# Kernel optimization log

Hardware: AMD Instinct MI355X
Metric: run time of the kernel (lower is better)

Reference implementation:

```python
import jax, jax.numpy as jnp
import numpy as np

NUM_HEADS = 16
FOCUS_FACTOR = 1.6
HEAD_REGION = {0: 0, 1: 1, 2: 2}  # head -> region (first/middle/end)


def setup_inputs() -> dict:
    key = jax.random.key(0)
    k1, k2, k3, k4, k5 = jax.random.split(key, 5)
    B, S, D = 2, 2048, 1024
    # GPT-2 style init scale so softmax is not fully saturated
    return {
        "hidden_states": jax.random.normal(k1, (B, S, D), dtype=jnp.float32),
        "c_attn_w": jax.random.normal(k2, (D, 3 * D), dtype=jnp.float32) * 0.02,
        "c_attn_b": jax.random.normal(k3, (3 * D,), dtype=jnp.float32) * 0.02,
        "c_proj_w": jax.random.normal(k4, (D, D), dtype=jnp.float32) * 0.02,
        "c_proj_b": jax.random.normal(k5, (D,), dtype=jnp.float32) * 0.02,
    }


def _region_multipliers(seq_len: int, num_heads: int, factor: float) -> jnp.ndarray:
    """[H, S] multiplier: selected heads up-weight their token region."""
    first_end = max(1, seq_len // 3)
    second_end = max(first_end + 1, 2 * seq_len // 3)
    pos = jnp.arange(seq_len)
    regions = [
        pos < first_end,
        (pos >= first_end) & (pos < second_end),
        pos >= second_end,
    ]
    mult = np.ones((num_heads, seq_len), dtype=np.float32)
    mult = jnp.asarray(mult)
    for h, r in HEAD_REGION.items():
        if h < num_heads:
            mult = mult.at[h].set(1.0 + (factor - 1.0) * regions[r].astype(jnp.float32))
    return mult


def reference(hidden_states, c_attn_w, c_attn_b, c_proj_w, c_proj_b):
    B, S, D = hidden_states.shape
    H = NUM_HEADS
    hd = D // H

    qkv = hidden_states @ c_attn_w + c_attn_b  # [B, S, 3D]
    q, k, v = jnp.split(qkv, 3, axis=-1)

    def _reshape(x):  # [B, S, D] -> [B, H, S, hd]
        return x.reshape(B, S, H, hd).transpose(0, 2, 1, 3)

    q, k, v = _reshape(q), _reshape(k), _reshape(v)

    scores = jnp.einsum("bhqd,bhkd->bhqk", q, k) / jnp.sqrt(jnp.float32(hd))
    causal = jnp.tril(jnp.ones((S, S), dtype=bool))
    mask_value = jnp.finfo(scores.dtype).min
    scores = jnp.where(causal[None, None], scores, mask_value)

    attn = jax.nn.softmax(scores, axis=-1)  # [B, H, S, S]

    # Per-head region reweight + renorm (only for the divergent heads)
    mult = _region_multipliers(S, H, FOCUS_FACTOR)  # [H, S]
    scaled = attn * mult[None, :, None, :]
    scaled = scaled / jnp.sum(scaled, axis=-1, keepdims=True)
    div_heads = jnp.zeros((H,), dtype=bool)
    for h in HEAD_REGION:
        if h < H:
            div_heads = div_heads.at[h].set(True)
    attn = jnp.where(div_heads[None, :, None, None], scaled, attn)

    out = jnp.einsum("bhqk,bhkd->bhqd", attn, v)  # [B, H, S, hd]
    out = out.transpose(0, 2, 1, 3).reshape(B, S, D)
    out = out @ c_proj_w + c_proj_b
    return out
```

## Files before the change

### kernel.cpp

```cpp
#include <hip/hip_runtime.h>
#include <hip/hip_bf16.h>

typedef __attribute__((ext_vector_type(8))) short bf16x8;
typedef __attribute__((ext_vector_type(4))) float f32x4;
typedef __attribute__((ext_vector_type(16))) float f32x16;
typedef __attribute__((ext_vector_type(4))) unsigned int u32x4;
typedef unsigned short u16;

#define MFMA_BF16(a, b, c) __builtin_amdgcn_mfma_f32_16x16x32_bf16(a, b, c, 0, 0, 0)
#define MFMA32(a, b, c) __builtin_amdgcn_mfma_f32_32x32x16_bf16(a, b, c, 0, 0, 0)

__device__ inline u16 f2b(float x) {
  unsigned int u = __builtin_bit_cast(unsigned int, x);
  u += 0x7fffu + ((u >> 16) & 1u);
  return (u16)(u >> 16);
}

__device__ inline float exp2_fast(float x) {
  float r;
  asm("v_exp_f32 %0, %1" : "=v"(r) : "v"(x));
  return r;
}

__device__ inline unsigned int cvtpk_bf16(float lo, float hi) {
  unsigned int r;
  asm("v_cvt_pk_bf16_f32 %0, %1, %2" : "=v"(r) : "v"(lo), "v"(hi));
  return r;
}

__device__ inline void pswap(unsigned int& dst, unsigned int& src) {
  asm("v_permlane32_swap_b32 %0, %1" : "+v"(dst), "+v"(src));
}

__device__ inline void gload16(void* lds, const void* g) {
  __builtin_amdgcn_global_load_lds((const __attribute__((address_space(1))) void*)g,
                                   (__attribute__((address_space(3))) void*)lds,
                                   16, 0, 0);
}


__global__ __launch_bounds__(256) void cast_f32_bf16(const float* __restrict__ src,
                                                     u16* __restrict__ dst, int n4) {
  int i = blockIdx.x * blockDim.x + threadIdx.x;
  if (i < n4) {
    float4 v = ((const float4*)src)[i];
    ushort4 o;
    o.x = f2b(v.x); o.y = f2b(v.y); o.z = f2b(v.z); o.w = f2b(v.w);
    ((ushort4*)dst)[i] = o;
  }
}

__global__ __launch_bounds__(256) void transpose_cast(const float* __restrict__ src,
                                                      u16* __restrict__ dst, int K, int N) {
  __shared__ float t[32][33];
  int k0 = blockIdx.x * 32, n0 = blockIdx.y * 32;
  int tx = threadIdx.x, ty = threadIdx.y;
#pragma unroll
  for (int i = 0; i < 4; i++) t[ty + i * 8][tx] = src[(size_t)(k0 + ty + i * 8) * N + n0 + tx];
  __syncthreads();
#pragma unroll
  for (int i = 0; i < 4; i++)
    dst[(size_t)(n0 + ty + i * 8) * K + k0 + tx] = f2b(t[tx][ty + i * 8]);
}

#define QSCALE 0.1803368801f

__global__ __launch_bounds__(512, 2) void gemm256_qkv(
    const u16* __restrict__ A, const u16* __restrict__ BT, const float* __restrict__ bias,
    u16* __restrict__ oQ, u16* __restrict__ oK, u16* __restrict__ oVf) {
  __shared__ __align__(16) u16 As[2][256 * 64];
  __shared__ __align__(16) u16 Bs[2][256 * 64];
  const int K = 1024, NT = 16;
  int tid = threadIdx.x;
  int wv = tid >> 6, lane = tid & 63, lr = lane & 15, lg = lane >> 4;
  int wm = wv >> 2, wn = wv & 3;
  int bx = blockIdx.x % 12, by = blockIdx.x / 12;
  int m0 = by * 256, n0 = bx * 256;
  const int swz = (lr & 7) << 4;

  f32x4 acc[8][4] = {};

  auto stageA = [&](int buf, int kt, int h) {
#pragma unroll
    for (int g = 0; g < 2; g++) {
      int li = g * 512 + tid;
      int row = (li >> 3) + h * 128;
      int cb = ((li & 7) * 16) ^ ((row & 7) << 4);
      gload16((char*)&As[buf][0] + h * 16384 + g * 8192 + wv * 1024,
              (const char*)(A + (size_t)(m0 + row) * K + kt * 64) + cb);
    }
  };
  auto stageB = [&](int buf, int kt, int h) {
#pragma unroll
    for (int g = 0; g < 2; g++) {
      int li = g * 512 + tid;
      int row = (li >> 3) + h * 128;
      int cb = ((li & 7) * 16) ^ ((row & 7) << 4);
      gload16((char*)&Bs[buf][0] + h * 16384 + g * 8192 + wv * 1024,
              (const char*)(BT + (size_t)(n0 + row) * K + kt * 64) + cb);
    }
  };

  stageA(0, 0, 0);
  stageB(0, 0, 0);
  stageA(0, 0, 1);
  stageB(0, 0, 1);

  for (int t = 0; t < NT; ++t) {
    const int buf = t & 1;
    const bool last = (t == NT - 1);
#pragma unroll
    for (int p = 0; p < 4; p++) {
      const int Mq = p & 1, Nq = p >> 1;
      if (last) {
        if (p == 0) asm volatile("s_waitcnt vmcnt(0)" ::: "memory");
      } else if (p < 3) {
        asm volatile("s_waitcnt vmcnt(4)" ::: "memory");
      }
      __builtin_amdgcn_s_barrier();
      bf16x8 a[4][2], b[2][2];
#pragma unroll
      for (int ii = 0; ii < 4; ii++) {
        int row = wm * 16 + ii * 32 + Mq * 128 + lr;
#pragma unroll
        for (int kk = 0; kk < 2; kk++)
          a[ii][kk] = *(const bf16x8*)((const char*)&As[buf][0] + row * 128 +
                                       ((kk * 64 + lg * 16) ^ swz));
      }
#pragma unroll
      for (int jj2 = 0; jj2 < 2; jj2++) {
        int row = wn * 16 + jj2 * 64 + Nq * 128 + lr;
#pragma unroll
        for (int kk = 0; kk < 2; kk++)
          b[jj2][kk] = *(const bf16x8*)((const char*)&Bs[buf][0] + row * 128 +
                                        ((kk * 64 + lg * 16) ^ swz));
      }
      if (!last) {
        if (p == 0) stageA(buf ^ 1, t + 1, 0);
        else if (p == 1) stageB(buf ^ 1, t + 1, 0);
        else if (p == 2) stageA(buf ^ 1, t + 1, 1);
        else stageB(buf ^ 1, t + 1, 1);
      }
      __builtin_amdgcn_s_setprio(1);
#pragma unroll
      for (int ii = 0; ii < 4; ii++)
#pragma unroll
        for (int jj2 = 0; jj2 < 2; jj2++)
#pragma unroll
          for (int kk = 0; kk < 2; kk++)
            acc[Mq * 4 + ii][Nq * 2 + jj2] =
                MFMA_BF16(a[ii][kk], b[jj2][kk], acc[Mq * 4 + ii][Nq * 2 + jj2]);
      __builtin_amdgcn_s_setprio(0);
    }
  }

#pragma unroll
  for (int i = 0; i < 8; i++) {
#pragma unroll
    for (int j = 0; j < 4; j++) {
#pragma unroll
      for (int jj = 0; jj < 4; jj++) {
        int row = m0 + wm * 16 + (i & 3) * 32 + (i >> 2) * 128 + lg * 4 + jj;
        int col = n0 + wn * 16 + (j & 1) * 64 + (j >> 1) * 128 + lr;
        float v = acc[i][j][jj] + bias[col];
        int bb = row >> 11, s = row & 2047;
        int tile = s >> 6, key = s & 63;
        if (col < 1024) {
          oQ[((size_t)((bb * 16 + (col >> 6)) * 2048 + s)) * 64 + (col & 63)] = f2b(v * QSCALE);
        } else if (col < 2048) {
          int c = col - 1024;
          int hh = c >> 6, d = c & 63;
          int jf = ((key >> 5) << 2) + (d >> 4);
          int ln = (((d >> 3) & 1) << 5) | (key & 31);
          oK[(size_t)(bb * 16 + hh) * 131072 + tile * 4096 + jf * 512 + ln * 8 + (d & 7)] =
              f2b(v);
        } else {
          int c = col - 2048;
          int hh = c >> 6, d = c & 63;
          int jf = ((d >> 5) << 2) + (key >> 4);
          int ln = (((key >> 3) & 1) << 5) | (d & 31);
          oVf[(size_t)(bb * 16 + hh) * 131072 + tile * 4096 + jf * 512 + ln * 8 + (key & 7)] =
              f2b(v);
        }
      }
    }
  }
}

__global__ __launch_bounds__(256) void gemm_bt_f32(
    const u16* __restrict__ A, const u16* __restrict__ BT, const float* __restrict__ bias,
    float* __restrict__ oF, int M, int N, int K, int nbx) {
  __shared__ __align__(16) u16 As[128 * 64];
  __shared__ __align__(16) u16 Bs[128 * 64];
  int tid = threadIdx.x;
  int wv = tid >> 6, lane = tid & 63, lr = lane & 15, lg = lane >> 4;
  int bx = blockIdx.x % nbx, by = blockIdx.x / nbx;
  int m0 = by * 128, n0 = bx * 128;
  int wr = (wv >> 1) * 64, wc = (wv & 1) * 64;

  f32x4 acc[4][4] = {};

  for (int k0 = 0; k0 < K; k0 += 64) {
#pragma unroll
    for (int j = 0; j < 4; j++) {
      int li = j * 256 + tid;
      int row = li >> 3;
      int cb = ((li & 7) * 16) ^ ((row & 7) << 4);
      gload16((char*)As + j * 4096 + wv * 1024,
              (const char*)(A + (size_t)(m0 + row) * K + k0) + cb);
      gload16((char*)Bs + j * 4096 + wv * 1024,
              (const char*)(BT + (size_t)(n0 + row) * K + k0) + cb);
    }
    __syncthreads();
#pragma unroll
    for (int kk = 0; kk < 2; kk++) {
      bf16x8 a[4], b[4];
#pragma unroll
      for (int i = 0; i < 4; i++) {
        int row = wr + i * 16 + lr;
        a[i] = *(const bf16x8*)((const char*)As + row * 128 +
                                ((kk * 64 + lg * 16) ^ ((row & 7) << 4)));
      }
#pragma unroll
      for (int j = 0; j < 4; j++) {
        int row = wc + j * 16 + lr;
        b[j] = *(const bf16x8*)((const char*)Bs + row * 128 +
                                ((kk * 64 + lg * 16) ^ ((row & 7) << 4)));
      }
#pragma unroll
      for (int i = 0; i < 4; i++)
#pragma unroll
        for (int j = 0; j < 4; j++) acc[i][j] = MFMA_BF16(a[i], b[j], acc[i][j]);
    }
    __syncthreads();
  }

#pragma unroll
  for (int i = 0; i < 4; i++)
#pragma unroll
    for (int j = 0; j < 4; j++)
#pragma unroll
      for (int jj = 0; jj < 4; jj++) {
        int row = m0 + wr + i * 16 + lg * 4 + jj;
        int col = n0 + wc + j * 16 + lr;
        oF[(size_t)row * N + col] = acc[i][j][jj] + bias[col];
      }
}

#define SEQL 2048
#define FIRST_END 682
#define SECOND_END 1365
#define LOG2F16 0.6780719051f

__global__ __launch_bounds__(256) void attn_kernel(const u16* __restrict__ Qb,
                                                   const u16* __restrict__ Kf,
                                                   const u16* __restrict__ Vf,
                                                   u16* __restrict__ AO) {
  __shared__ float Ol[4][16][66];
  __shared__ float Ml[4][32], Ll[4][32], Cl[4][32];

  int tid = threadIdx.x;
  int w = tid >> 6, l = tid & 63;
  int r31 = l & 31, hi = l >> 5;

  int xcd = blockIdx.x & 7, slot = blockIdx.x >> 3;
  int bh = xcd * 4 + (slot >> 6);
  int qt = 63 - (slot & 63);
  int q0 = qt * 32;
  int h = bh & 15, b = bh >> 4;

  const u16* Qp = Qb + ((size_t)bh * SEQL + q0 + r31) * 64 + hi * 8;
  bf16x8 qa[4];
#pragma unroll
  for (int kb = 0; kb < 4; kb++) qa[kb] = *(const bf16x8*)(Qp + kb * 16);

  const u16* Kfp = Kf + (size_t)bh * 131072;
  const u16* Vfp = Vf + (size_t)bh * 131072;

  f32x16 o0 = {}, o1 = {};
  float m = -1e30f, lsum = 0.f;

  const int N = (q0 + 95) >> 6;
  const bool hasb = (h < 3);

  for (int t = w; t < N; t += 4) {
    const int kv0 = t << 6;
    const bool last = (t == N - 1);
    const u16* kt = Kfp + (size_t)t * 4096;
    const u16* vt = Vfp + (size_t)t * 4096;

    bf16x8 ka[4], kb2[4];
#pragma unroll
    for (int kb = 0; kb < 4; kb++) {
      ka[kb]  = *(const bf16x8*)(kt + kb * 512 + l * 8);
      kb2[kb] = *(const bf16x8*)(kt + (4 + kb) * 512 + l * 8);
    }
    f32x16 sA = {}, sB = {};
#pragma unroll
    for (int kb = 0; kb < 4; kb++) sA = MFMA32(ka[kb], qa[kb], sA);
#pragma unroll
    for (int kb = 0; kb < 4; kb++) sB = MFMA32(kb2[kb], qa[kb], sB);

    if (hasb) {
#pragma unroll
      for (int r = 0; r < 16; r++) {
        int kA = kv0 + ((r & 3) + 8 * (r >> 2) + 4 * hi);
        int kB = kA + 32;
        int rA = (kA < FIRST_END) ? 0 : (kA < SECOND_END) ? 1 : 2;
        int rB = (kB < FIRST_END) ? 0 : (kB < SECOND_END) ? 1 : 2;
        if (rA == h) sA[r] += LOG2F16;
        if (rB == h) sB[r] += LOG2F16;
      }
    }
    if (last) {
      int q = q0 + r31;
#pragma unroll
      for (int r = 0; r < 16; r++) {
        int kA = kv0 + ((r & 3) + 8 * (r >> 2) + 4 * hi);
        if (kA > q) sA[r] = -1e30f;
        if (kA + 32 > q) sB[r] = -1e30f;
      }
    }

#define MAX4(v, i) fmaxf(fmaxf(v[i], v[i + 1]), fmaxf(v[i + 2], v[i + 3]))
    float mA = fmaxf(fmaxf(MAX4(sA, 0), MAX4(sA, 4)), fmaxf(MAX4(sA, 8), MAX4(sA, 12)));
    float mB = fmaxf(fmaxf(MAX4(sB, 0), MAX4(sB, 4)), fmaxf(MAX4(sB, 8), MAX4(sB, 12)));
    float mx = fmaxf(mA, mB);
    mx = fmaxf(mx, __shfl_xor(mx, 32));
    float mn = fmaxf(m, mx);
    float corr = exp2_fast(m - mn);
    m = mn;

    unsigned int wA[8], wB[8];
    float s0 = 0.f, s1 = 0.f;
#pragma unroll
    for (int i = 0; i < 8; i++) {
      float pa0 = exp2_fast(sA[2 * i] - mn), pa1 = exp2_fast(sA[2 * i + 1] - mn);
      float pb0 = exp2_fast(sB[2 * i] - mn), pb1 = exp2_fast(sB[2 * i + 1] - mn);
      s0 += pa0 + pa1;
      s1 += pb0 + pb1;
      wA[i] = cvtpk_bf16(pa0, pa1);
      wB[i] = cvtpk_bf16(pb0, pb1);
    }
    float ssum = s0 + s1;
    ssum += __shfl_xor(ssum, 32);
    lsum = lsum * corr + ssum;
    o0 *= corr;
    o1 *= corr;

    pswap(wA[0], wA[2]); pswap(wA[1], wA[3]);
    pswap(wA[4], wA[6]); pswap(wA[5], wA[7]);
    pswap(wB[0], wB[2]); pswap(wB[1], wB[3]);
    pswap(wB[4], wB[6]); pswap(wB[5], wB[7]);

    bf16x8 pb[4];
    pb[0] = __builtin_bit_cast(bf16x8, (u32x4){wA[0], wA[1], wA[2], wA[3]});
    pb[1] = __builtin_bit_cast(bf16x8, (u32x4){wA[4], wA[5], wA[6], wA[7]});
    pb[2] = __builtin_bit_cast(bf16x8, (u32x4){wB[0], wB[1], wB[2], wB[3]});
    pb[3] = __builtin_bit_cast(bf16x8, (u32x4){wB[4], wB[5], wB[6], wB[7]});

#pragma unroll
    for (int c = 0; c < 4; c++) {
      bf16x8 va0 = *(const bf16x8*)(vt + c * 512 + l * 8);
      bf16x8 va1 = *(const bf16x8*)(vt + (4 + c) * 512 + l * 8);
      o0 = MFMA32(va0, pb[c], o0);
      o1 = MFMA32(va1, pb[c], o1);
    }
  }

  Ml[w][r31] = m;
  Ll[w][r31] = lsum;
#pragma unroll
  for (int r = 0; r < 16; r++) Ol[w][r][l] = o0[r];
  __syncthreads();

  if (tid < 128) {
    int w2 = tid >> 5, q = tid & 31;
    float m0 = Ml[0][q], m1 = Ml[1][q], m2 = Ml[2][q], m3 = Ml[3][q];
    float ms = fmaxf(fmaxf(m0, m1), fmaxf(m2, m3));
    float e0 = exp2_fast(m0 - ms), e1 = exp2_fast(m1 - ms);
    float e2 = exp2_fast(m2 - ms), e3 = exp2_fast(m3 - ms);
    float ls = Ll[0][q] * e0 + Ll[1][q] * e1 + Ll[2][q] * e2 + Ll[3][q] * e3;
    float ei = (w2 == 0) ? e0 : (w2 == 1) ? e1 : (w2 == 2) ? e2 : e3;
    Cl[w2][q] = ei / ls;
  }
  __syncthreads();

  int mq = tid >> 3, md = (tid & 7) * 4;
  float c0 = Cl[0][mq], c1 = Cl[1][mq], c2 = Cl[2][mq], c3 = Cl[3][mq];
  u16* aop = AO + ((size_t)(b * SEQL + q0 + mq)) * 1024 + h * 64;

  {
    u16 ov[4];
#pragma unroll
    for (int j = 0; j < 4; j++) {
      int d = md + j;
      int h2 = (d >> 2) & 1, rr = (d & 3) + 4 * (d >> 3);
      int ll2 = mq + 32 * h2;
      ov[j] = f2b(Ol[0][rr][ll2] * c0 + Ol[1][rr][ll2] * c1 +
                  Ol[2][rr][ll2] * c2 + Ol[3][rr][ll2] * c3);
    }
    *(uint2*)(aop + md) = *(const uint2*)ov;
  }
  __syncthreads();
#pragma unroll
  for (int r = 0; r < 16; r++) Ol[w][r][l] = o1[r];
  __syncthreads();
  {
    u16 ov[4];
#pragma unroll
    for (int j = 0; j < 4; j++) {
      int d = md + j;
      int h2 = (d >> 2) & 1, rr = (d & 3) + 4 * (d >> 3);
      int ll2 = mq + 32 * h2;
      ov[j] = f2b(Ol[0][rr][ll2] * c0 + Ol[1][rr][ll2] * c1 +
                  Ol[2][rr][ll2] * c2 + Ol[3][rr][ll2] * c3);
    }
    *(uint2*)(aop + 32 + md) = *(const uint2*)ov;
  }
}


extern "C" void kernel_launch(void* const* d_in, const int* in_sizes, int n_in,
                              void* d_out, int out_size, void* d_ws, size_t ws_size,
                              hipStream_t stream) {
  const float* hs = (const float*)d_in[0];
  const float* w1 = (const float*)d_in[1];
  const float* b1 = (const float*)d_in[2];
  const float* w2 = (const float*)d_in[3];
  const float* b2 = (const float*)d_in[4];
  float* out = (float*)d_out;

  char* ws = (char*)d_ws;
  const size_t MB = 1u << 20;
  u16* hsb = (u16*)(ws + 0);
  u16* w1t = (u16*)(ws + 8 * MB);
  u16* w2t = (u16*)(ws + 14 * MB);
  u16* Qb = (u16*)(ws + 16 * MB);
  u16* Kf = (u16*)(ws + 24 * MB);
  u16* Vf = (u16*)(ws + 32 * MB);
  u16* AO = hsb;

  cast_f32_bf16<<<4096, 256, 0, stream>>>(hs, hsb, 4096 * 1024 / 4);
  dim3 tb(32, 8);
  transpose_cast<<<dim3(32, 96), tb, 0, stream>>>(w1, w1t, 1024, 3072);
  transpose_cast<<<dim3(32, 32), tb, 0, stream>>>(w2, w2t, 1024, 1024);

  gemm256_qkv<<<16 * 12, 512, 0, stream>>>(hsb, w1t, b1, Qb, Kf, Vf);
  attn_kernel<<<2048, 256, 0, stream>>>(Qb, Kf, Vf, AO);
  gemm_bt_f32<<<32 * 8, 256, 0, stream>>>(AO, w2t, b2, out, 4096, 1024, 1024, 8);
}
```

Before: 130.6 us.

## Share double-buffered LDS K/V tiles across four query waves in attention

Each attention block now covers 128 queries, one 32-query slice per wave, instead of 32 queries with the KV range split across waves. K/V tiles are staged into a double-buffered LDS area with direct global-to-LDS loads, so all four waves reuse each tile and the next tile is prefetched during compute. This removes the cross-wave softmax merge through shared memory and lets each wave write its normalized output directly. The trade-off is four times fewer blocks and waves, longer serial KV loops per wave, and barrier-induced idling from causal imbalance between waves in the same block.

```diff
diff --git a/kernel.cpp b/kernel.cpp
--- a/kernel.cpp
+++ b/kernel.cpp
@@ -252,21 +252,21 @@
 #define SECOND_END 1365
 #define LOG2F16 0.6780719051f
 
-__global__ __launch_bounds__(256) void attn_kernel(const u16* __restrict__ Qb,
-                                                   const u16* __restrict__ Kf,
-                                                   const u16* __restrict__ Vf,
-                                                   u16* __restrict__ AO) {
-  __shared__ float Ol[4][16][66];
-  __shared__ float Ml[4][32], Ll[4][32], Cl[4][32];
+__global__ __launch_bounds__(256, 2) void attn_kernel(const u16* __restrict__ Qb,
+                                                      const u16* __restrict__ Kf,
+                                                      const u16* __restrict__ Vf,
+                                                      u16* __restrict__ AO) {
+  __shared__ __align__(16) char KV[2][16384];
 
   int tid = threadIdx.x;
   int w = tid >> 6, l = tid & 63;
   int r31 = l & 31, hi = l >> 5;
 
   int xcd = blockIdx.x & 7, slot = blockIdx.x >> 3;
-  int bh = xcd * 4 + (slot >> 6);
-  int qt = 63 - (slot & 63);
-  int q0 = qt * 32;
+  int bh = xcd * 4 + (slot & 3);
+  int qb = 15 - (slot >> 2);
+  int q0B = qb * 128;
+  int q0 = q0B + w * 32;
   int h = bh & 15, b = bh >> 4;
 
   const u16* Qp = Qb + ((size_t)bh * SEQL + q0 + r31) * 64 + hi * 8;
@@ -274,149 +274,134 @@
 #pragma unroll
   for (int kb = 0; kb < 4; kb++) qa[kb] = *(const bf16x8*)(Qp + kb * 16);
 
-  const u16* Kfp = Kf + (size_t)bh * 131072;
-  const u16* Vfp = Vf + (size_t)bh * 131072;
+  const char* Ktg = (const char*)(Kf + (size_t)bh * 131072);
+  const char* Vtg = (const char*)(Vf + (size_t)bh * 131072);
 
   f32x16 o0 = {}, o1 = {};
   float m = -1e30f, lsum = 0.f;
 
-  const int N = (q0 + 95) >> 6;
+  const int nsteps_w = (q0 + 95) >> 6;
+  const int nsteps_blk = (q0B + 191) >> 6;
   const bool hasb = (h < 3);
 
-  for (int t = w; t < N; t += 4) {
-    const int kv0 = t << 6;
-    const bool last = (t == N - 1);
-    const u16* kt = Kfp + (size_t)t * 4096;
-    const u16* vt = Vfp + (size_t)t * 4096;
-
-    bf16x8 ka[4], kb2[4];
-#pragma unroll
-    for (int kb = 0; kb < 4; kb++) {
-      ka[kb]  = *(const bf16x8*)(kt + kb * 512 + l * 8);
-      kb2[kb] = *(const bf16x8*)(kt + (4 + kb) * 512 + l * 8);
-    }
-    f32x16 sA = {}, sB = {};
-#pragma unroll
-    for (int kb = 0; kb < 4; kb++) sA = MFMA32(ka[kb], qa[kb], sA);
-#pragma unroll
-    for (int kb = 0; kb < 4; kb++) sB = MFMA32(kb2[kb], qa[kb], sB);
-
-    if (hasb) {
-#pragma unroll
-      for (int r = 0; r < 16; r++) {
-        int kA = kv0 + ((r & 3) + 8 * (r >> 2) + 4 * hi);
-        int kB = kA + 32;
-        int rA = (kA < FIRST_END) ? 0 : (kA < SECOND_END) ? 1 : 2;
-        int rB = (kB < FIRST_END) ? 0 : (kB < SECOND_END) ? 1 : 2;
-        if (rA == h) sA[r] += LOG2F16;
-        if (rB == h) sB[r] += LOG2F16;
-      }
-    }
-    if (last) {
-      int q = q0 + r31;
-#pragma unroll
-      for (int r = 0; r < 16; r++) {
-        int kA = kv0 + ((r & 3) + 8 * (r >> 2) + 4 * hi);
-        if (kA > q) sA[r] = -1e30f;
-        if (kA + 32 > q) sB[r] = -1e30f;
-      }
-    }
+  auto stage = [&](int buf, int t) {
+    const char* ks = Ktg + (size_t)t * 8192;
+    const char* vs = Vtg + (size_t)t * 8192;
+#pragma unroll
+    for (int r = 0; r < 2; r++) {
+      gload16(&KV[buf][r * 4096 + w * 1024], ks + r * 4096 + w * 1024 + l * 16);
+      gload16(&KV[buf][8192 + r * 4096 + w * 1024], vs + r * 4096 + w * 1024 + l * 16);
+    }
+  };
+
+  stage(0, 0);
+  asm volatile("s_waitcnt vmcnt(0)" ::: "memory");
+  __builtin_amdgcn_s_barrier();
+
+  for (int t = 0; t < nsteps_blk; ++t) {
+    const int cur = t & 1;
+    if (t + 1 < nsteps_blk) stage(cur ^ 1, t + 1);
+
+    if (t < nsteps_w) {
+      const int kv0 = t << 6;
+      const bool last = (t == nsteps_w - 1);
+      const char* kt = &KV[cur][0];
+      const char* vt = &KV[cur][8192];
+
+      bf16x8 ka[4], kb2[4];
+#pragma unroll
+      for (int kb = 0; kb < 4; kb++) {
+        ka[kb]  = *(const bf16x8*)(kt + kb * 1024 + l * 16);
+        kb2[kb] = *(const bf16x8*)(kt + (4 + kb) * 1024 + l * 16);
+      }
+      f32x16 sA = {}, sB = {};
+#pragma unroll
+      for (int kb = 0; kb < 4; kb++) sA = MFMA32(ka[kb], qa[kb], sA);
+#pragma unroll
+      for (int kb = 0; kb < 4; kb++) sB = MFMA32(kb2[kb], qa[kb], sB);
+
+      if (hasb) {
+#pragma unroll
+        for (int r = 0; r < 16; r++) {
+          int kA = kv0 + ((r & 3) + 8 * (r >> 2) + 4 * hi);
+          int kB = kA + 32;
+          int rA = (kA < FIRST_END) ? 0 : (kA < SECOND_END) ? 1 : 2;
+          int rB = (kB < FIRST_END) ? 0 : (kB < SECOND_END) ? 1 : 2;
+          if (rA == h) sA[r] += LOG2F16;
+          if (rB == h) sB[r] += LOG2F16;
+        }
+      }
+      if (last) {
+        int q = q0 + r31;
+#pragma unroll
+        for (int r = 0; r < 16; r++) {
+          int kA = kv0 + ((r & 3) + 8 * (r >> 2) + 4 * hi);
+          if (kA > q) sA[r] = -1e30f;
+          if (kA + 32 > q) sB[r] = -1e30f;
+        }
+      }
 
 #define MAX4(v, i) fmaxf(fmaxf(v[i], v[i + 1]), fmaxf(v[i + 2], v[i + 3]))
-    float mA = fmaxf(fmaxf(MAX4(sA, 0), MAX4(sA, 4)), fmaxf(MAX4(sA, 8), MAX4(sA, 12)));
-    float mB = fmaxf(fmaxf(MAX4(sB, 0), MAX4(sB, 4)), fmaxf(MAX4(sB, 8), MAX4(sB, 12)));
-    float mx = fmaxf(mA, mB);
-    mx = fmaxf(mx, __shfl_xor(mx, 32));
-    float mn = fmaxf(m, mx);
-    float corr = exp2_fast(m - mn);
-    m = mn;
-
-    unsigned int wA[8], wB[8];
-    float s0 = 0.f, s1 = 0.f;
-#pragma unroll
-    for (int i = 0; i < 8; i++) {
-      float pa0 = exp2_fast(sA[2 * i] - mn), pa1 = exp2_fast(sA[2 * i + 1] - mn);
-      float pb0 = exp2_fast(sB[2 * i] - mn), pb1 = exp2_fast(sB[2 * i + 1] - mn);
-      s0 += pa0 + pa1;
-      s1 += pb0 + pb1;
-      wA[i] = cvtpk_bf16(pa0, pa1);
-      wB[i] = cvtpk_bf16(pb0, pb1);
-    }
-    float ssum = s0 + s1;
-    ssum += __shfl_xor(ssum, 32);
-    lsum = lsum * corr + ssum;
-    o0 *= corr;
-    o1 *= corr;
-
-    pswap(wA[0], wA[2]); pswap(wA[1], wA[3]);
-    pswap(wA[4], wA[6]); pswap(wA[5], wA[7]);
-    pswap(wB[0], wB[2]); pswap(wB[1], wB[3]);
-    pswap(wB[4], wB[6]); pswap(wB[5], wB[7]);
-
-    bf16x8 pb[4];
-    pb[0] = __builtin_bit_cast(bf16x8, (u32x4){wA[0], wA[1], wA[2], wA[3]});
-    pb[1] = __builtin_bit_cast(bf16x8, (u32x4){wA[4], wA[5], wA[6], wA[7]});
-    pb[2] = __builtin_bit_cast(bf16x8, (u32x4){wB[0], wB[1], wB[2], wB[3]});
-    pb[3] = __builtin_bit_cast(bf16x8, (u32x4){wB[4], wB[5], wB[6], wB[7]});
-
-#pragma unroll
-    for (int c = 0; c < 4; c++) {
-      bf16x8 va0 = *(const bf16x8*)(vt + c * 512 + l * 8);
-      bf16x8 va1 = *(const bf16x8*)(vt + (4 + c) * 512 + l * 8);
-      o0 = MFMA32(va0, pb[c], o0);
-      o1 = MFMA32(va1, pb[c], o1);
-    }
-  }
-
-  Ml[w][r31] = m;
-  Ll[w][r31] = lsum;
-#pragma unroll
-  for (int r = 0; r < 16; r++) Ol[w][r][l] = o0[r];
-  __syncthreads();
-
-  if (tid < 128) {
-    int w2 = tid >> 5, q = tid & 31;
-    float m0 = Ml[0][q], m1 = Ml[1][q], m2 = Ml[2][q], m3 = Ml[3][q];
-    float ms = fmaxf(fmaxf(m0, m1), fmaxf(m2, m3));
-    float e0 = exp2_fast(m0 - ms), e1 = exp2_fast(m1 - ms);
-    float e2 = exp2_fast(m2 - ms), e3 = exp2_fast(m3 - ms);
-    float ls = Ll[0][q] * e0 + Ll[1][q] * e1 + Ll[2][q] * e2 + Ll[3][q] * e3;
-    float ei = (w2 == 0) ? e0 : (w2 == 1) ? e1 : (w2 == 2) ? e2 : e3;
-    Cl[w2][q] = ei / ls;
-  }
-  __syncthreads();
-
-  int mq = tid >> 3, md = (tid & 7) * 4;
-  float c0 = Cl[0][mq], c1 = Cl[1][mq], c2 = Cl[2][mq], c3 = Cl[3][mq];
-  u16* aop = AO + ((size_t)(b * SEQL + q0 + mq)) * 1024 + h * 64;
-
-  {
-    u16 ov[4];
-#pragma unroll
-    for (int j = 0; j < 4; j++) {
-      int d = md + j;
-      int h2 = (d >> 2) & 1, rr = (d & 3) + 4 * (d >> 3);
-      int ll2 = mq + 32 * h2;
-      ov[j] = f2b(Ol[0][rr][ll2] * c0 + Ol[1][rr][ll2] * c1 +
-                  Ol[2][rr][ll2] * c2 + Ol[3][rr][ll2] * c3);
-    }
-    *(uint2*)(aop + md) = *(const uint2*)ov;
-  }
-  __syncthreads();
-#pragma unroll
-  for (int r = 0; r < 16; r++) Ol[w][r][l] = o1[r];
-  __syncthreads();
-  {
-    u16 ov[4];
-#pragma unroll
-    for (int j = 0; j < 4; j++) {
-      int d = md + j;
-      int h2 = (d >> 2) & 1, rr = (d & 3) + 4 * (d >> 3);
-      int ll2 = mq + 32 * h2;
-      ov[j] = f2b(Ol[0][rr][ll2] * c0 + Ol[1][rr][ll2] * c1 +
-                  Ol[2][rr][ll2] * c2 + Ol[3][rr][ll2] * c3);
-    }
-    *(uint2*)(aop + 32 + md) = *(const uint2*)ov;
+      float mA = fmaxf(fmaxf(MAX4(sA, 0), MAX4(sA, 4)), fmaxf(MAX4(sA, 8), MAX4(sA, 12)));
+      float mB = fmaxf(fmaxf(MAX4(sB, 0), MAX4(sB, 4)), fmaxf(MAX4(sB, 8), MAX4(sB, 12)));
+      float mx = fmaxf(mA, mB);
+      mx = fmaxf(mx, __shfl_xor(mx, 32));
+      float mn = fmaxf(m, mx);
+      float corr = exp2_fast(m - mn);
+      m = mn;
+
+      unsigned int wA[8], wB[8];
+      float s0 = 0.f, s1 = 0.f;
+#pragma unroll
+      for (int i = 0; i < 8; i++) {
+        float pa0 = exp2_fast(sA[2 * i] - mn), pa1 = exp2_fast(sA[2 * i + 1] - mn);
+        float pb0 = exp2_fast(sB[2 * i] - mn), pb1 = exp2_fast(sB[2 * i + 1] - mn);
+        s0 += pa0 + pa1;
+        s1 += pb0 + pb1;
+        wA[i] = cvtpk_bf16(pa0, pa1);
+        wB[i] = cvtpk_bf16(pb0, pb1);
+      }
+      float ssum = s0 + s1;
+      ssum += __shfl_xor(ssum, 32);
+      lsum = lsum * corr + ssum;
+      o0 *= corr;
+      o1 *= corr;
+
+      pswap(wA[0], wA[2]); pswap(wA[1], wA[3]);
+      pswap(wA[4], wA[6]); pswap(wA[5], wA[7]);
+      pswap(wB[0], wB[2]); pswap(wB[1], wB[3]);
+      pswap(wB[4], wB[6]); pswap(wB[5], wB[7]);
+
+      bf16x8 pb[4];
+      pb[0] = __builtin_bit_cast(bf16x8, (u32x4){wA[0], wA[1], wA[2], wA[3]});
+      pb[1] = __builtin_bit_cast(bf16x8, (u32x4){wA[4], wA[5], wA[6], wA[7]});
+      pb[2] = __builtin_bit_cast(bf16x8, (u32x4){wB[0], wB[1], wB[2], wB[3]});
+      pb[3] = __builtin_bit_cast(bf16x8, (u32x4){wB[4], wB[5], wB[6], wB[7]});
+
+#pragma unroll
+      for (int c = 0; c < 4; c++) {
+        bf16x8 va0 = *(const bf16x8*)(vt + c * 1024 + l * 16);
+        bf16x8 va1 = *(const bf16x8*)(vt + (4 + c) * 1024 + l * 16);
+        o0 = MFMA32(va0, pb[c], o0);
+        o1 = MFMA32(va1, pb[c], o1);
+      }
+    }
+
+    asm volatile("s_waitcnt vmcnt(0)" ::: "memory");
+    __builtin_amdgcn_s_barrier();
+  }
+
+  float inv = 1.0f / lsum;
+  u16* aop = AO + ((size_t)(b * SEQL + q0 + r31)) * 1024 + h * 64;
+#pragma unroll
+  for (int dt = 0; dt < 2; dt++) {
+    const f32x16& o = dt ? o1 : o0;
+#pragma unroll
+    for (int r = 0; r < 16; r += 2) {
+      int d = dt * 32 + (r & 3) + 8 * (r >> 2) + 4 * hi;
+      unsigned int wo = (unsigned int)f2b(o[r] * inv) | ((unsigned int)f2b(o[r + 1] * inv) << 16);
+      *(unsigned int*)(aop + d) = wo;
+    }
   }
 }
 
@@ -447,6 +432,6 @@
   transpose_cast<<<dim3(32, 32), tb, 0, stream>>>(w2, w2t, 1024, 1024);
 
   gemm256_qkv<<<16 * 12, 512, 0, stream>>>(hsb, w1t, b1, Qb, Kf, Vf);
-  attn_kernel<<<2048, 256, 0, stream>>>(Qb, Kf, Vf, AO);
+  attn_kernel<<<512, 256, 0, stream>>>(Qb, Kf, Vf, AO);
   gemm_bt_f32<<<32 * 8, 256, 0, stream>>>(AO, w2t, b2, out, 4096, 1024, 1024, 8);
 }
```

Measured after the change: 146.3 us. 1.12x slower.

## Switch QKV GEMM to 32x32x16 MFMA with two-phase staging schedule

Applied to the files above, without the earlier changes.

Rewrites the 256x256 QKV projection GEMM inner loop to use 32x32x16 bf16 MFMA tiles instead of 16x16x32, so each wave holds 4x2 blocks of 32x32 accumulators. The k-loop now has two barrier phases per tile instead of four, and global prefetch of the next tile is interleaved between MFMA groups in a new order (A0, B0, B1, A1). The larger MFMA shape raises operand reuse per LDS read and cuts barrier count. The epilogue index mapping is changed to match the 32x32 accumulator layout, and the waitcnt thresholds are retuned for the new load order, which carries some risk of ordering mistakes.

```diff
diff --git a/kernel.cpp b/kernel.cpp
--- a/kernel.cpp
+++ b/kernel.cpp
@@ -72,13 +72,13 @@
   __shared__ __align__(16) u16 Bs[2][256 * 64];
   const int K = 1024, NT = 16;
   int tid = threadIdx.x;
-  int wv = tid >> 6, lane = tid & 63, lr = lane & 15, lg = lane >> 4;
+  int wv = tid >> 6, lane = tid & 63;
+  int r31 = lane & 31, hi = lane >> 5;
   int wm = wv >> 2, wn = wv & 3;
   int bx = blockIdx.x % 12, by = blockIdx.x / 12;
   int m0 = by * 256, n0 = bx * 256;
-  const int swz = (lr & 7) << 4;
-
-  f32x4 acc[8][4] = {};
+
+  f32x16 acc[4][2] = {};
 
   auto stageA = [&](int buf, int kt, int h) {
 #pragma unroll
@@ -103,66 +103,87 @@
 
   stageA(0, 0, 0);
   stageB(0, 0, 0);
+  stageB(0, 0, 1);
   stageA(0, 0, 1);
-  stageB(0, 0, 1);
 
   for (int t = 0; t < NT; ++t) {
     const int buf = t & 1;
     const bool last = (t == NT - 1);
-#pragma unroll
-    for (int p = 0; p < 4; p++) {
-      const int Mq = p & 1, Nq = p >> 1;
-      if (last) {
-        if (p == 0) asm volatile("s_waitcnt vmcnt(0)" ::: "memory");
-      } else if (p < 3) {
-        asm volatile("s_waitcnt vmcnt(4)" ::: "memory");
-      }
-      __builtin_amdgcn_s_barrier();
-      bf16x8 a[4][2], b[2][2];
-#pragma unroll
-      for (int ii = 0; ii < 4; ii++) {
-        int row = wm * 16 + ii * 32 + Mq * 128 + lr;
-#pragma unroll
-        for (int kk = 0; kk < 2; kk++)
-          a[ii][kk] = *(const bf16x8*)((const char*)&As[buf][0] + row * 128 +
-                                       ((kk * 64 + lg * 16) ^ swz));
-      }
-#pragma unroll
-      for (int jj2 = 0; jj2 < 2; jj2++) {
-        int row = wn * 16 + jj2 * 64 + Nq * 128 + lr;
-#pragma unroll
-        for (int kk = 0; kk < 2; kk++)
-          b[jj2][kk] = *(const bf16x8*)((const char*)&Bs[buf][0] + row * 128 +
-                                        ((kk * 64 + lg * 16) ^ swz));
-      }
-      if (!last) {
-        if (p == 0) stageA(buf ^ 1, t + 1, 0);
-        else if (p == 1) stageB(buf ^ 1, t + 1, 0);
-        else if (p == 2) stageA(buf ^ 1, t + 1, 1);
-        else stageB(buf ^ 1, t + 1, 1);
-      }
-      __builtin_amdgcn_s_setprio(1);
-#pragma unroll
-      for (int ii = 0; ii < 4; ii++)
-#pragma unroll
-        for (int jj2 = 0; jj2 < 2; jj2++)
-#pragma unroll
-          for (int kk = 0; kk < 2; kk++)
-            acc[Mq * 4 + ii][Nq * 2 + jj2] =
-                MFMA_BF16(a[ii][kk], b[jj2][kk], acc[Mq * 4 + ii][Nq * 2 + jj2]);
-      __builtin_amdgcn_s_setprio(0);
-    }
-  }
-
-#pragma unroll
-  for (int i = 0; i < 8; i++) {
-#pragma unroll
-    for (int j = 0; j < 4; j++) {
-#pragma unroll
-      for (int jj = 0; jj < 4; jj++) {
-        int row = m0 + wm * 16 + (i & 3) * 32 + (i >> 2) * 128 + lg * 4 + jj;
-        int col = n0 + wn * 16 + (j & 1) * 64 + (j >> 1) * 128 + lr;
-        float v = acc[i][j][jj] + bias[col];
+    const char* Ab = (const char*)&As[buf][0];
+    const char* Bb = (const char*)&Bs[buf][0];
+    bf16x8 a[2][4], b[2][4];
+
+    asm volatile("s_waitcnt vmcnt(2)" ::: "memory");
+    __builtin_amdgcn_s_barrier();
+#pragma unroll
+    for (int i = 0; i < 2; i++) {
+      int row = (wm + 2 * i) * 32 + r31;
+#pragma unroll
+      for (int kk = 0; kk < 4; kk++)
+        a[i][kk] = *(const bf16x8*)(Ab + row * 128 + ((kk * 32 + hi * 16) ^ ((row & 7) << 4)));
+    }
+#pragma unroll
+    for (int nb = 0; nb < 2; nb++) {
+      int row = (wn + 4 * nb) * 32 + r31;
+#pragma unroll
+      for (int kk = 0; kk < 4; kk++)
+        b[nb][kk] = *(const bf16x8*)(Bb + row * 128 + ((kk * 32 + hi * 16) ^ ((row & 7) << 4)));
+    }
+    if (!last) stageA(buf ^ 1, t + 1, 0);
+    __builtin_amdgcn_s_setprio(1);
+#pragma unroll
+    for (int i = 0; i < 2; i++)
+#pragma unroll
+      for (int kk = 0; kk < 4; kk++) acc[i][0] = MFMA32(a[i][kk], b[0][kk], acc[i][0]);
+    __builtin_amdgcn_s_setprio(0);
+
+    if (!last) stageB(buf ^ 1, t + 1, 0);
+    __builtin_amdgcn_s_setprio(1);
+#pragma unroll
+    for (int i = 0; i < 2; i++)
+#pragma unroll
+      for (int kk = 0; kk < 4; kk++) acc[i][1] = MFMA32(a[i][kk], b[1][kk], acc[i][1]);
+    __builtin_amdgcn_s_setprio(0);
+
+    if (last) {
+      asm volatile("s_waitcnt vmcnt(0)" ::: "memory");
+    } else {
+      asm volatile("s_waitcnt vmcnt(4)" ::: "memory");
+    }
+    __builtin_amdgcn_s_barrier();
+#pragma unroll
+    for (int i = 0; i < 2; i++) {
+      int row = (wm + 2 * (2 + i)) * 32 + r31;
+#pragma unroll
+      for (int kk = 0; kk < 4; kk++)
+        a[i][kk] = *(const bf16x8*)(Ab + row * 128 + ((kk * 32 + hi * 16) ^ ((row & 7) << 4)));
+    }
+    if (!last) stageB(buf ^ 1, t + 1, 1);
+    __builtin_amdgcn_s_setprio(1);
+#pragma unroll
+    for (int i = 0; i < 2; i++)
+#pragma unroll
+      for (int kk = 0; kk < 4; kk++) acc[2 + i][0] = MFMA32(a[i][kk], b[0][kk], acc[2 + i][0]);
+    __builtin_amdgcn_s_setprio(0);
+
+    if (!last) stageA(buf ^ 1, t + 1, 1);
+    __builtin_amdgcn_s_setprio(1);
+#pragma unroll
+    for (int i = 0; i < 2; i++)
+#pragma unroll
+      for (int kk = 0; kk < 4; kk++) acc[2 + i][1] = MFMA32(a[i][kk], b[1][kk], acc[2 + i][1]);
+    __builtin_amdgcn_s_setprio(0);
+  }
+
+#pragma unroll
+  for (int mb = 0; mb < 4; mb++) {
+#pragma unroll
+    for (int nb = 0; nb < 2; nb++) {
+#pragma unroll
+      for (int r = 0; r < 16; r++) {
+        int row = m0 + (wm + 2 * mb) * 32 + (r & 3) + 8 * (r >> 2) + 4 * hi;
+        int col = n0 + (wn + 4 * nb) * 32 + r31;
+        float v = acc[mb][nb][r] + bias[col];
         int bb = row >> 11, s = row & 2047;
         int tile = s >> 6, key = s & 63;
         if (col < 1024) {
```

Result: slower. 135.4 us (+3.7%).

## Restructure QKV GEMM main loop into unrolled two-tile pipelined phases

Applied to the files above, without the earlier changes.

Rewrites the QKV projection GEMM loop so two K tiles are processed per iteration in eight explicit macro phases. Each phase loads LDS fragments, issues half-tile global stages for future tiles, and then runs its MFMAs. Staging of the other buffer is split across phases, with explicit vmcnt waits and double barriers per phase. The aim is deeper prefetch and better overlap of global loads with MFMA work, at the cost of more barriers and more complex buffer-hazard ordering.

```diff
diff --git a/kernel.cpp b/kernel.cpp
--- a/kernel.cpp
+++ b/kernel.cpp
@@ -65,18 +65,46 @@
 
 #define QSCALE 0.1803368801f
 
+#define GPHASE(MQ, NQ, BUF, STAGE, GATE)                                               \
+  do {                                                                                 \
+    bf16x8 a[4][2], b[2][2];                                                           \
+    _Pragma("unroll") for (int ii = 0; ii < 4; ii++) {                                 \
+      int row = wm * 16 + ii * 32 + MQ * 128 + lr;                                     \
+      _Pragma("unroll") for (int kk = 0; kk < 2; kk++)                                 \
+          a[ii][kk] = *(const bf16x8*)((const char*)&As[BUF][0] + row * 128 +          \
+                                       ((kk * 64 + lg * 16) ^ ((row & 7) << 4)));      \
+    }                                                                                  \
+    _Pragma("unroll") for (int jj2 = 0; jj2 < 2; jj2++) {                              \
+      int row = wn * 16 + jj2 * 64 + NQ * 128 + lr;                                    \
+      _Pragma("unroll") for (int kk = 0; kk < 2; kk++)                                 \
+          b[jj2][kk] = *(const bf16x8*)((const char*)&Bs[BUF][0] + row * 128 +         \
+                                        ((kk * 64 + lg * 16) ^ ((row & 7) << 4)));     \
+    }                                                                                  \
+    STAGE;                                                                             \
+    __builtin_amdgcn_s_barrier();                                                      \
+    __builtin_amdgcn_s_setprio(1);                                                     \
+    _Pragma("unroll") for (int ii = 0; ii < 4; ii++)                                   \
+        _Pragma("unroll") for (int jj2 = 0; jj2 < 2; jj2++)                            \
+            _Pragma("unroll") for (int kk = 0; kk < 2; kk++)                           \
+                acc[MQ * 4 + ii][NQ * 2 + jj2] =                                       \
+        MFMA_BF16(a[ii][kk], b[jj2][kk], acc[MQ * 4 + ii][NQ * 2 + jj2]);              \
+    __builtin_amdgcn_s_setprio(0);                                                     \
+    GATE;                                                                              \
+    __builtin_amdgcn_sched_barrier(0);                                                 \
+    __builtin_amdgcn_s_barrier();                                                      \
+  } while (0)
+
 __global__ __launch_bounds__(512, 2) void gemm256_qkv(
     const u16* __restrict__ A, const u16* __restrict__ BT, const float* __restrict__ bias,
     u16* __restrict__ oQ, u16* __restrict__ oK, u16* __restrict__ oVf) {
   __shared__ __align__(16) u16 As[2][256 * 64];
   __shared__ __align__(16) u16 Bs[2][256 * 64];
-  const int K = 1024, NT = 16;
+  const int K = 1024;
   int tid = threadIdx.x;
   int wv = tid >> 6, lane = tid & 63, lr = lane & 15, lg = lane >> 4;
   int wm = wv >> 2, wn = wv & 3;
   int bx = blockIdx.x % 12, by = blockIdx.x / 12;
   int m0 = by * 256, n0 = bx * 256;
-  const int swz = (lr & 7) << 4;
 
   f32x4 acc[8][4] = {};
 
@@ -101,57 +129,28 @@
     }
   };
 
-  stageA(0, 0, 0);
-  stageB(0, 0, 0);
-  stageA(0, 0, 1);
-  stageB(0, 0, 1);
-
-  for (int t = 0; t < NT; ++t) {
-    const int buf = t & 1;
-    const bool last = (t == NT - 1);
-#pragma unroll
-    for (int p = 0; p < 4; p++) {
-      const int Mq = p & 1, Nq = p >> 1;
-      if (last) {
-        if (p == 0) asm volatile("s_waitcnt vmcnt(0)" ::: "memory");
-      } else if (p < 3) {
-        asm volatile("s_waitcnt vmcnt(4)" ::: "memory");
-      }
-      __builtin_amdgcn_s_barrier();
-      bf16x8 a[4][2], b[2][2];
-#pragma unroll
-      for (int ii = 0; ii < 4; ii++) {
-        int row = wm * 16 + ii * 32 + Mq * 128 + lr;
-#pragma unroll
-        for (int kk = 0; kk < 2; kk++)
-          a[ii][kk] = *(const bf16x8*)((const char*)&As[buf][0] + row * 128 +
-                                       ((kk * 64 + lg * 16) ^ swz));
-      }
-#pragma unroll
-      for (int jj2 = 0; jj2 < 2; jj2++) {
-        int row = wn * 16 + jj2 * 64 + Nq * 128 + lr;
-#pragma unroll
-        for (int kk = 0; kk < 2; kk++)
-          b[jj2][kk] = *(const bf16x8*)((const char*)&Bs[buf][0] + row * 128 +
-                                        ((kk * 64 + lg * 16) ^ swz));
-      }
-      if (!last) {
-        if (p == 0) stageA(buf ^ 1, t + 1, 0);
-        else if (p == 1) stageB(buf ^ 1, t + 1, 0);
-        else if (p == 2) stageA(buf ^ 1, t + 1, 1);
-        else stageB(buf ^ 1, t + 1, 1);
-      }
-      __builtin_amdgcn_s_setprio(1);
-#pragma unroll
-      for (int ii = 0; ii < 4; ii++)
-#pragma unroll
-        for (int jj2 = 0; jj2 < 2; jj2++)
-#pragma unroll
-          for (int kk = 0; kk < 2; kk++)
-            acc[Mq * 4 + ii][Nq * 2 + jj2] =
-                MFMA_BF16(a[ii][kk], b[jj2][kk], acc[Mq * 4 + ii][Nq * 2 + jj2]);
-      __builtin_amdgcn_s_setprio(0);
-    }
+  stageA(0, 0, 0); stageB(0, 0, 0); stageA(0, 0, 1); stageB(0, 0, 1);
+  stageB(1, 1, 0); stageA(1, 1, 0); stageA(1, 1, 1); stageB(1, 1, 1);
+  asm volatile("s_waitcnt vmcnt(8)" ::: "memory");
+  __builtin_amdgcn_s_barrier();
+
+  for (int i = 0; i < 8; ++i) {
+    const int t1 = 2 * i + 1, t2 = 2 * i + 2, t3 = 2 * i + 3;
+    const bool s01 = (i > 0);
+    const bool s36 = (i < 7);
+    const bool s78 = (i < 7);
+
+    GPHASE(0, 0, 0, if (s01) stageA(1, t1, 1), );
+    GPHASE(1, 0, 0, if (s01) stageB(1, t1, 1), );
+    GPHASE(0, 1, 0, if (s36) stageB(0, t2, 0), );
+    GPHASE(1, 1, 0, if (s36) stageA(0, t2, 0),
+           if (i == 7) { asm volatile("s_waitcnt vmcnt(0)" ::: "memory"); }
+           else { asm volatile("s_waitcnt vmcnt(4)" ::: "memory"); });
+    GPHASE(0, 0, 1, if (s36) stageA(0, t2, 1), );
+    GPHASE(1, 0, 1, if (s36) stageB(0, t2, 1), );
+    GPHASE(0, 1, 1, if (s78) stageB(1, t3, 0), );
+    GPHASE(1, 1, 1, if (s78) stageA(1, t3, 0),
+           if (i < 7) { asm volatile("s_waitcnt vmcnt(4)" ::: "memory"); });
   }
 
 #pragma unroll
```

After: 137.1 us. +5.0%, slower.
